# Optimization experiments

Measured on AMD Instinct MI355X. Metric: run time of the kernel, lower is better.

Reference implementation:

```python
import jax, jax.numpy as jnp
import numpy as np

D_MODEL = 1024
NUM_HEADS = 16
HEAD_DIM = D_MODEL // NUM_HEADS


def setup_inputs() -> dict:
    key = jax.random.key(0)
    ks = jax.random.split(key, 11)
    B, S = 2, 2048
    s = 1.0 / np.sqrt(D_MODEL)
    inp = {
        'q': jax.random.normal(ks[0], (B, S, D_MODEL), jnp.float32),
        'k': jax.random.normal(ks[1], (B, S, D_MODEL), jnp.float32),
        'v': jax.random.normal(ks[2], (B, S, D_MODEL), jnp.float32),
        'wq': jax.random.normal(ks[3], (D_MODEL, D_MODEL), jnp.float32) * s,
        'bq': jnp.zeros((D_MODEL,), jnp.float32),
        'wk': jax.random.normal(ks[4], (D_MODEL, D_MODEL), jnp.float32) * s,
        'bk': jnp.zeros((D_MODEL,), jnp.float32),
        'wv': jax.random.normal(ks[5], (D_MODEL, D_MODEL), jnp.float32) * s,
        'bv': jnp.zeros((D_MODEL,), jnp.float32),
        'wo': jax.random.normal(ks[6], (D_MODEL, D_MODEL), jnp.float32) * s,
        'bo': jnp.zeros((D_MODEL,), jnp.float32),
    }
    return inp


def _split_heads(x, B):
    # [B, S, D] -> [B, H, S, Hd]
    return x.reshape(B, -1, NUM_HEADS, HEAD_DIM).transpose(0, 2, 1, 3)


def reference(q, k, v, wq, bq, wk, bk, wv, bv, wo, bo):
    B = q.shape[0]
    qh = _split_heads(q @ wq + bq, B)
    kh = _split_heads(k @ wk + bk, B)
    vh = _split_heads(v @ wv + bv, B)
    scale = 1.0 / np.sqrt(HEAD_DIM).astype(np.float32)
    # [B, H, Sq, Sk]
    scores = jnp.einsum('bhqd,bhkd->bhqk', qh, kh) * scale
    probs = jax.nn.softmax(scores, axis=-1)
    out = jnp.einsum('bhqk,bhkd->bhqd', probs, vh)  # [B, H, Sq, Hd]
    out = out.transpose(0, 2, 1, 3).reshape(B, -1, D_MODEL)
    return out @ wo + bo
```

## Files before the change

kernel.cpp:

```cpp
#include <hip/hip_runtime.h>

typedef unsigned short u16;
typedef __bf16 bf16x8 __attribute__((ext_vector_type(8)));
typedef float    f32x4 __attribute__((ext_vector_type(4)));
typedef float   f32x16 __attribute__((ext_vector_type(16)));
typedef u16      u16x8 __attribute__((ext_vector_type(8)));
typedef u16      u16x4 __attribute__((ext_vector_type(4)));
typedef unsigned uint4v __attribute__((ext_vector_type(4)));

#define DM 1024
#define SQ 2048
#define HD 64
#define QSCALE 0.18033688f

#define SWZ8(row, ch) ((((ch) ^ ((row) & 7) ^ ((row) >> 3)) & 7))

__device__ __forceinline__ u16 f2bf(float f) {
    unsigned u = __builtin_bit_cast(unsigned, f);
    u += 0x7FFFu + ((u >> 16) & 1u);
    return (u16)(u >> 16);
}

__device__ __forceinline__ bf16x8 ldsbf(const u16* p) {
    return __builtin_bit_cast(bf16x8, *(const u16x8*)p);
}

__device__ __forceinline__ unsigned cvtpk(float a, float b) {
    unsigned r;
    asm("v_cvt_pk_bf16_f32 %0, %1, %2" : "=v"(r) : "v"(a), "v"(b));
    return r;
}

__device__ __forceinline__ void swap32(unsigned &a, unsigned &b) {
    asm volatile("v_permlane32_swap_b32 %0, %1" : "+v"(a), "+v"(b));
}

typedef __attribute__((address_space(3))) unsigned lds_u32_t;
typedef __attribute__((address_space(1))) const unsigned glob_u32_t;
__device__ __forceinline__ void gl_lds16(const u16* g, u16* l) {
    __builtin_amdgcn_global_load_lds((glob_u32_t*)g, (lds_u32_t*)l, 16, 0, 0);
}

__global__ __launch_bounds__(256) void convert_kernel(
    const float* __restrict__ q, const float* __restrict__ k,
    const float* __restrict__ v,
    u16* __restrict__ Qc, u16* __restrict__ Kc, u16* __restrict__ Vc)
{
    const int which = blockIdx.x >> 11;
    const float* src = (which==0) ? q : (which==1) ? k : v;
    u16* dst         = (which==0) ? Qc : (which==1) ? Kc : Vc;
    const int off = ((blockIdx.x & 2047) << 11) + threadIdx.x * 8;
    f32x4 x0 = *(const f32x4*)&src[off];
    f32x4 x1 = *(const f32x4*)&src[off + 4];
    u16x8 u;
#pragma unroll
    for (int e = 0; e < 4; ++e) { u[e] = f2bf(x0[e]); u[e+4] = f2bf(x1[e]); }
    *(u16x8*)&dst[off] = u;
}

__global__ __launch_bounds__(256) void wtrans_kernel(
    const float* __restrict__ w0, const float* __restrict__ w1,
    const float* __restrict__ w2, const float* __restrict__ w3,
    u16* __restrict__ t0, u16* __restrict__ t1,
    u16* __restrict__ t2, u16* __restrict__ t3)
{
    __shared__ float tile[32][33];
    const int z = blockIdx.z;
    const float* W = (z==0) ? w0 : (z==1) ? w1 : (z==2) ? w2 : w3;
    u16* T        = (z==0) ? t0 : (z==1) ? t1 : (z==2) ? t2 : t3;
    const float sc = (z==0) ? QSCALE : 1.0f;
    const int tx = threadIdx.x & 31, ty = threadIdx.x >> 5;
    const int n0 = blockIdx.x * 32, k0 = blockIdx.y * 32;
#pragma unroll
    for (int i = 0; i < 4; ++i)
        tile[ty + 8*i][tx] = W[(size_t)(k0 + ty + 8*i)*DM + n0 + tx];
    __syncthreads();
#pragma unroll
    for (int i = 0; i < 4; ++i)
        T[(size_t)(n0 + ty + 8*i)*DM + k0 + tx] = f2bf(tile[tx][ty + 8*i] * sc);
}

template<bool OF32, bool VTLAST>
__global__ __launch_bounds__(256) void gemm_kernel(
    const u16* __restrict__ a0, const u16* __restrict__ a1, const u16* __restrict__ a2,
    const u16* __restrict__ w0, const u16* __restrict__ w1, const u16* __restrict__ w2,
    const float* __restrict__ bi0, const float* __restrict__ bi1, const float* __restrict__ bi2,
    void* __restrict__ o0, void* __restrict__ o1, void* __restrict__ o2,
    float bscale0)
{
    __shared__ __align__(16) u16 As[128*64];
    __shared__ __align__(16) u16 Bs[128*64];

    const int cpx  = gridDim.x >> 3;
    const int wgid = (blockIdx.x & 7) * cpx + (blockIdx.x >> 3);
    const int z   = wgid >> 8;
    const int rem = wgid & 255;
    const int by  = rem >> 3, bx = rem & 7;

    const u16*  Ap  = (z==0) ? a0 : (z==1) ? a1 : a2;
    const u16*  Wp  = (z==0) ? w0 : (z==1) ? w1 : w2;
    const float* Bp = (z==0) ? bi0 : (z==1) ? bi1 : bi2;
    void* Op        = (z==0) ? o0 : (z==1) ? o1 : o2;
    const float bsc = (z==0) ? bscale0 : 1.0f;

    const int tid  = threadIdx.x;
    const int lane = tid & 63;
    const int wv   = tid >> 6;
    const int m0 = by * 128;
    const int n0 = bx * 128;
    const int wr = (wv >> 1) * 64;
    const int wc = (wv & 1) * 64;
    const int g  = lane >> 4;
    const int mm = lane & 15;

    const int l8  = lane >> 3;
    const int chs = (lane & 7) ^ l8;
    const int lrow = wv*8 + l8;

    const f32x4 zero4 = {0.f, 0.f, 0.f, 0.f};
    f32x4 acc[4][4];
#pragma unroll
    for (int i = 0; i < 4; ++i)
#pragma unroll
        for (int j = 0; j < 4; ++j) acc[i][j] = zero4;

    for (int kt = 0; kt < 16; ++kt) {
        const int k0 = kt * 64;
#pragma unroll
        for (int i = 0; i < 4; ++i) {
            const int row = i*32 + lrow;
            gl_lds16(&Ap[(size_t)(m0+row)*DM + k0 + chs*8], &As[(i*32 + wv*8)*64]);
            gl_lds16(&Wp[(size_t)(n0+row)*DM + k0 + chs*8], &Bs[(i*32 + wv*8)*64]);
        }
        __syncthreads();
#pragma unroll
        for (int ks = 0; ks < 2; ++ks) {
            bf16x8 af[4], bfr[4];
#pragma unroll
            for (int rt = 0; rt < 4; ++rt) {
                const int row = wr + rt*16 + mm;
                const int ch  = ks*4 + g;
                af[rt] = ldsbf(&As[row*64 + ((ch ^ (row & 7)) << 3)]);
            }
#pragma unroll
            for (int ct = 0; ct < 4; ++ct) {
                const int row = wc + ct*16 + mm;
                const int ch  = ks*4 + g;
                bfr[ct] = ldsbf(&Bs[row*64 + ((ch ^ (row & 7)) << 3)]);
            }
            __builtin_amdgcn_s_setprio(1);
#pragma unroll
            for (int rt = 0; rt < 4; ++rt)
#pragma unroll
                for (int ct = 0; ct < 4; ++ct)
                    acc[rt][ct] = __builtin_amdgcn_mfma_f32_16x16x32_bf16(
                        af[rt], bfr[ct], acc[rt][ct], 0, 0, 0);
            __builtin_amdgcn_s_setprio(0);
        }
        __syncthreads();
    }
    if (VTLAST && z == 2) {
#pragma unroll
        for (int ct = 0; ct < 4; ++ct) {
            const int col = n0 + wc + ct*16 + mm;
            const float bv = Bp[col] * bsc;
#pragma unroll
            for (int rt = 0; rt < 4; ++rt) {
                const int row0 = m0 + wr + rt*16 + g*4;
                const int bb = row0 >> 11, s = row0 & (SQ-1);
                u16x4 pk;
#pragma unroll
                for (int r = 0; r < 4; ++r) pk[r] = f2bf(acc[rt][ct][r] + bv);
                *(u16x4*)&((u16*)Op)[(size_t)(bb*DM + col)*SQ + s] = pk;
            }
        }
    } else {
#pragma unroll
        for (int ct = 0; ct < 4; ++ct) {
            const int col = n0 + wc + ct*16 + mm;
            const float bv = Bp[col] * bsc;
#pragma unroll
            for (int rt = 0; rt < 4; ++rt) {
#pragma unroll
                for (int r = 0; r < 4; ++r) {
                    const int row = m0 + wr + rt*16 + g*4 + r;
                    const float vv = acc[rt][ct][r] + bv;
                    if (OF32) ((float*)Op)[(size_t)row*DM + col] = vv;
                    else      ((u16*) Op)[(size_t)row*DM + col] = f2bf(vv);
                }
            }
        }
    }
}

__global__ __launch_bounds__(256) void attn_kernel(
    const u16* __restrict__ Q, const u16* __restrict__ K,
    const u16* __restrict__ Vt, u16* __restrict__ Z)
{
    __shared__ __align__(16) u16 Kl[2][64*64];
    __shared__ __align__(16) u16 Vl[2][64*64];

    const int tid  = threadIdx.x;
    const int lane = tid & 63;
    const int wid  = tid >> 6;
    const int c    = lane & 31;
    const int hi   = lane >> 5;
    const int srow = tid >> 3;
    const int c8   = tid & 7;

    const int wg = (blockIdx.x & 7) * 64 + (blockIdx.x >> 3);
    const int qt = wg & 15;
    const int hb = wg >> 4;
    const int h  = hb & 15;
    const int b  = hb >> 4;
    const int q0 = qt * 128;

    const size_t kbase = (size_t)(b*SQ)*DM + h*HD;
    const size_t vbase = (size_t)((b*16 + h)*HD)*SQ;

    bf16x8 qf[4];
    {
        const size_t qoff = (size_t)(b*SQ + q0 + wid*32 + c)*DM + h*HD + hi*8;
#pragma unroll
        for (int ks = 0; ks < 4; ++ks)
            qf[ks] = ldsbf(&Q[qoff + ks*16]);
    }

    f32x16 oacc[2];
#pragma unroll
    for (int dt = 0; dt < 2; ++dt)
#pragma unroll
        for (int r = 0; r < 16; ++r) oacc[dt][r] = 0.f;
    f32x16 z16;
#pragma unroll
    for (int r = 0; r < 16; ++r) z16[r] = 0.f;
    float lsum = 0.f;

    int stw[2];
    u16x8 kreg[2], vreg[2];
#pragma unroll
    for (int p = 0; p < 2; ++p) {
        const int row = p*32 + srow;
        stw[p] = row*64 + (SWZ8(row, c8) << 3);
        kreg[p] = *(const u16x8*)&K [kbase + (size_t)row*DM + c8*8];
        vreg[p] = *(const u16x8*)&Vt[vbase + (size_t)row*SQ + c8*8];
        *(u16x8*)&Kl[0][stw[p]] = kreg[p];
        *(u16x8*)&Vl[0][stw[p]] = vreg[p];
    }

    for (int t = 0; t < SQ/64; ++t) {
        const int cur = t & 1;
        if (t + 1 < SQ/64) {
#pragma unroll
            for (int p = 0; p < 2; ++p) {
                const int row = p*32 + srow;
                kreg[p] = *(const u16x8*)&K [kbase + (size_t)((t+1)*64 + row)*DM + c8*8];
                vreg[p] = *(const u16x8*)&Vt[vbase + (size_t)row*SQ + (t+1)*64 + c8*8];
            }
        }
        __syncthreads();

        f32x16 pacc[2];
        __builtin_amdgcn_s_setprio(1);
#pragma unroll
        for (int kt = 0; kt < 2; ++kt) {
            const int row = kt*32 + c;
            bf16x8 kf = ldsbf(&Kl[cur][row*64 + (SWZ8(row, hi) << 3)]);
            pacc[kt] = __builtin_amdgcn_mfma_f32_32x32x16_bf16(kf, qf[0], z16, 0, 0, 0);
        }
#pragma unroll
        for (int ks = 1; ks < 4; ++ks) {
#pragma unroll
            for (int kt = 0; kt < 2; ++kt) {
                const int row = kt*32 + c;
                const int ch  = ks*2 + hi;
                bf16x8 kf = ldsbf(&Kl[cur][row*64 + (SWZ8(row, ch) << 3)]);
                pacc[kt] = __builtin_amdgcn_mfma_f32_32x32x16_bf16(kf, qf[ks], pacc[kt], 0, 0, 0);
            }
        }
        __builtin_amdgcn_s_setprio(0);

        float ls = 0.f;
#pragma unroll
        for (int kt = 0; kt < 2; ++kt)
#pragma unroll
            for (int r = 0; r < 16; ++r) {
                const float e = __builtin_amdgcn_exp2f(pacc[kt][r]);
                pacc[kt][r] = e;
                ls += e;
            }
        lsum += ls;

        bf16x8 pa[4];
#pragma unroll
        for (int kt = 0; kt < 2; ++kt)
#pragma unroll
            for (int k2 = 0; k2 < 2; ++k2) {
                const int bs = k2*8;
                unsigned u = cvtpk(pacc[kt][bs+0], pacc[kt][bs+1]);
                unsigned v = cvtpk(pacc[kt][bs+2], pacc[kt][bs+3]);
                unsigned w = cvtpk(pacc[kt][bs+4], pacc[kt][bs+5]);
                unsigned x = cvtpk(pacc[kt][bs+6], pacc[kt][bs+7]);
                swap32(u, w);
                swap32(v, x);
                uint4v fr = {u, v, w, x};
                pa[kt*2 + k2] = __builtin_bit_cast(bf16x8, fr);
            }

        __builtin_amdgcn_s_setprio(1);
#pragma unroll
        for (int kp = 0; kp < 4; ++kp) {
#pragma unroll
            for (int dt = 0; dt < 2; ++dt) {
                const int d  = dt*32 + c;
                const int ch = kp*2 + hi;
                bf16x8 vf = ldsbf(&Vl[cur][d*64 + (SWZ8(d, ch) << 3)]);
                oacc[dt] = __builtin_amdgcn_mfma_f32_32x32x16_bf16(pa[kp], vf, oacc[dt], 0, 0, 0);
            }
        }
        __builtin_amdgcn_s_setprio(0);

        if (t + 1 < SQ/64) {
#pragma unroll
            for (int p = 0; p < 2; ++p) {
                *(u16x8*)&Kl[cur^1][stw[p]] = kreg[p];
                *(u16x8*)&Vl[cur^1][stw[p]] = vreg[p];
            }
        }
    }

    lsum += __shfl_xor(lsum, 32, 64);
    const float linv = 1.f / lsum;
    float linvr[16];
#pragma unroll
    for (int r = 0; r < 16; ++r)
        linvr[r] = __shfl(linv, (r & 3) + 8*(r >> 2) + 4*hi, 64);

#pragma unroll
    for (int dt = 0; dt < 2; ++dt)
#pragma unroll
        for (int r = 0; r < 16; ++r) {
            const int qrl = (r & 3) + 8*(r >> 2) + 4*hi;
            const size_t row = (size_t)(b*SQ + q0 + wid*32 + qrl);
            Z[row*DM + h*HD + dt*32 + c] = f2bf(oacc[dt][r] * linvr[r]);
        }
}

extern "C" void kernel_launch(void* const* d_in, const int* in_sizes, int n_in,
                              void* d_out, int out_size, void* d_ws, size_t ws_size,
                              hipStream_t stream)
{
    const float* q  = (const float*)d_in[0];
    const float* k  = (const float*)d_in[1];
    const float* v  = (const float*)d_in[2];
    const float* wq = (const float*)d_in[3];
    const float* bq = (const float*)d_in[4];
    const float* wk = (const float*)d_in[5];
    const float* bk = (const float*)d_in[6];
    const float* wv = (const float*)d_in[7];
    const float* bv = (const float*)d_in[8];
    const float* wo = (const float*)d_in[9];
    const float* bo = (const float*)d_in[10];
    float* out = (float*)d_out;

    char* ws = (char*)d_ws;
    u16* Qc  = (u16*)(ws);
    u16* Kc  = (u16*)(ws + 8388608);
    u16* Vc  = (u16*)(ws + 16777216);
    u16* Qb  = (u16*)(ws + 25165824);
    u16* Kb  = (u16*)(ws + 33554432);
    u16* VtB = (u16*)(ws + 41943040);
    u16* WtQ = (u16*)(ws + 50331648);
    u16* WtK = (u16*)(ws + 52428800);
    u16* WtV = (u16*)(ws + 54525952);
    u16* WtO = (u16*)(ws + 56623104);
    u16* Zb  = Qc;

    wtrans_kernel<<<dim3(32, 32, 4), 256, 0, stream>>>(
        wq, wk, wv, wo, WtQ, WtK, WtV, WtO);

    convert_kernel<<<dim3(3*2048), 256, 0, stream>>>(q, k, v, Qc, Kc, Vc);

    gemm_kernel<false, true><<<dim3(768), 256, 0, stream>>>(
        Qc, Kc, Vc, WtQ, WtK, WtV, bq, bk, bv,
        (void*)Qb, (void*)Kb, (void*)VtB, QSCALE);

    attn_kernel<<<dim3(512), 256, 0, stream>>>(Qb, Kb, VtB, Zb);

    gemm_kernel<true, false><<<dim3(256), 256, 0, stream>>>(
        Zb, Zb, Zb, WtO, WtO, WtO, bo, bo, bo,
        (void*)out, (void*)out, (void*)out, 1.0f);
}
```

Before: 131.3 us.

## Stage K/V tiles via direct global-to-LDS loads and split softmax row-sum accumulators

Replaces the register-staged K/V prefetch (global load into registers, then LDS store after compute) with direct global-to-LDS loads issued right after the barrier into the other buffer. The swizzle moves to the global address side so the LDS layout stays the same. This drops the VGPRs and ds_write work spent on staging. It also splits the exp row-sum into four partial accumulators to shorten the dependent add chain. The risk is correctness: the async LDS writes must be complete before the next barrier and reads, and gl_lds16 is assumed to be defined in the hidden code.

```diff
diff --git a/kernel.cpp b/kernel.cpp
--- a/kernel.cpp
+++ b/kernel.cpp
@@ -205,8 +205,9 @@
     const int wid  = tid >> 6;
     const int c    = lane & 31;
     const int hi   = lane >> 5;
-    const int srow = tid >> 3;
-    const int c8   = tid & 7;
+    const int l8   = lane >> 3;
+    const int c8l  = lane & 7;
+    const int rb   = wid*8 + l8;
 
     const int wg = (blockIdx.x & 7) * 64 + (blockIdx.x >> 3);
     const int qt = wg & 15;
@@ -234,31 +235,26 @@
     f32x16 z16;
 #pragma unroll
     for (int r = 0; r < 16; ++r) z16[r] = 0.f;
-    float lsum = 0.f;
-
-    int stw[2];
-    u16x8 kreg[2], vreg[2];
-#pragma unroll
-    for (int p = 0; p < 2; ++p) {
-        const int row = p*32 + srow;
-        stw[p] = row*64 + (SWZ8(row, c8) << 3);
-        kreg[p] = *(const u16x8*)&K [kbase + (size_t)row*DM + c8*8];
-        vreg[p] = *(const u16x8*)&Vt[vbase + (size_t)row*SQ + c8*8];
-        *(u16x8*)&Kl[0][stw[p]] = kreg[p];
-        *(u16x8*)&Vl[0][stw[p]] = vreg[p];
-    }
+    float lsp[4] = {0.f, 0.f, 0.f, 0.f};
+
+    auto stage = [&](int tt, int buf) {
+#pragma unroll
+        for (int p = 0; p < 2; ++p) {
+            const int row = p*32 + rb;
+            const int ch  = (c8l ^ (row & 7) ^ (row >> 3)) & 7;
+            gl_lds16(&K [kbase + (size_t)(tt*64 + row)*DM + ch*8],
+                     &Kl[buf][(p*32 + wid*8)*64]);
+            gl_lds16(&Vt[vbase + (size_t)row*SQ + tt*64 + ch*8],
+                     &Vl[buf][(p*32 + wid*8)*64]);
+        }
+    };
+
+    stage(0, 0);
 
     for (int t = 0; t < SQ/64; ++t) {
         const int cur = t & 1;
-        if (t + 1 < SQ/64) {
-#pragma unroll
-            for (int p = 0; p < 2; ++p) {
-                const int row = p*32 + srow;
-                kreg[p] = *(const u16x8*)&K [kbase + (size_t)((t+1)*64 + row)*DM + c8*8];
-                vreg[p] = *(const u16x8*)&Vt[vbase + (size_t)row*SQ + (t+1)*64 + c8*8];
-            }
-        }
         __syncthreads();
+        if (t + 1 < SQ/64) stage(t+1, cur^1);
 
         f32x16 pacc[2];
         __builtin_amdgcn_s_setprio(1);
@@ -280,16 +276,14 @@
         }
         __builtin_amdgcn_s_setprio(0);
 
-        float ls = 0.f;
 #pragma unroll
         for (int kt = 0; kt < 2; ++kt)
 #pragma unroll
             for (int r = 0; r < 16; ++r) {
                 const float e = __builtin_amdgcn_exp2f(pacc[kt][r]);
                 pacc[kt][r] = e;
-                ls += e;
-            }
-        lsum += ls;
+                lsp[r & 3] += e;
+            }
 
         bf16x8 pa[4];
 #pragma unroll
@@ -319,16 +313,9 @@
             }
         }
         __builtin_amdgcn_s_setprio(0);
-
-        if (t + 1 < SQ/64) {
-#pragma unroll
-            for (int p = 0; p < 2; ++p) {
-                *(u16x8*)&Kl[cur^1][stw[p]] = kreg[p];
-                *(u16x8*)&Vl[cur^1][stw[p]] = vreg[p];
-            }
-        }
     }
 
+    float lsum = (lsp[0] + lsp[1]) + (lsp[2] + lsp[3]);
     lsum += __shfl_xor(lsum, 32, 64);
     const float linv = 1.f / lsum;
     float linvr[16];
```

After: 135.0 us. 1.03x slower.
